# Performance work log

Measured on AMD Instinct MI355X. Metric: run time of the kernel, lower is better.

## Reference

```python
import jax, jax.numpy as jnp
import numpy as np
import math

NUM_HEADS = 8
HEAD_DIM = 64
MID = NUM_HEADS * HEAD_DIM  # 512
OUT_FEATURES = 512
NUM_BUCKETS = 32            # rel_pos_num_buckets (module passes 2*this to bucket fn)
MAX_DISTANCE = 128
SCALE = HEAD_DIM ** -0.5


def _relative_position_bucket(rel_pos, num_buckets, max_distance):
    # faithful port of RelativePositionBias._relative_position_bucket
    num_buckets = num_buckets // 2
    ret = (rel_pos >= 0).astype(jnp.int32) * num_buckets
    n = jnp.abs(rel_pos)
    max_exact = max(1, num_buckets // 2)
    denom = math.log(max_distance / max_exact) if max_distance > max_exact else 1.0
    n_float = jnp.maximum(n.astype(jnp.float32), 1.0)
    val_if_large = (max_exact + jnp.log(n_float / max_exact) / denom * (num_buckets - max_exact)).astype(jnp.int32)
    val_if_large = jnp.minimum(val_if_large, num_buckets - 1)
    ret = ret + jnp.where(n < max_exact, n, val_if_large)
    return ret


def rel_pos_bias(table, num_q, num_k):
    # table: [2*NUM_BUCKETS, heads] -> bias [1, heads, q, k]
    q_pos = jnp.arange(num_q, dtype=jnp.int32)
    k_pos = jnp.arange(num_k, dtype=jnp.int32)
    rel = k_pos[None, :] - q_pos[:, None]                      # [q, k]
    bucket = _relative_position_bucket(rel, NUM_BUCKETS * 2, MAX_DISTANCE)
    bias = table[bucket]                                       # [q, k, h]
    return jnp.transpose(bias, (2, 0, 1))[None]                # [1, h, q, k]


def setup_inputs() -> dict:
    key = jax.random.key(0)
    ks = jax.random.split(key, 6)
    b, n = 2, 4096
    q = jax.random.normal(ks[0], (b, n, MID), dtype=jnp.float32)
    k = jax.random.normal(ks[1], (b, n, MID), dtype=jnp.float32)
    v = jax.random.normal(ks[2], (b, n, MID), dtype=jnp.float32)
    # bucket indices range over [0, 2*NUM_BUCKETS); size table accordingly
    rel_bias_table = jax.random.normal(ks[3], (2 * NUM_BUCKETS, NUM_HEADS), dtype=jnp.float32) * 0.02
    W_out = jax.random.normal(ks[4], (MID, OUT_FEATURES), dtype=jnp.float32) * (1.0 / math.sqrt(MID))
    b_out = jax.random.normal(ks[5], (OUT_FEATURES,), dtype=jnp.float32) * 0.01
    return {"q": q, "k": k, "v": v, "rel_bias_table": rel_bias_table, "W_out": W_out, "b_out": b_out}


def reference(q, k, v, rel_bias_table, W_out, b_out):
    b, n, _ = q.shape
    m = k.shape[1]
    split = lambda t: jnp.transpose(t.reshape(t.shape[0], t.shape[1], NUM_HEADS, HEAD_DIM), (0, 2, 1, 3))
    qh, kh, vh = split(q), split(k), split(v)                  # [b, h, n, d]
    sim = jnp.einsum('bhnd,bhmd->bhnm', qh, kh)                # [b, h, n, m]
    sim = sim + rel_pos_bias(rel_bias_table, n, m)             # bias added BEFORE scaling (as in source)
    sim = sim * SCALE
    attn = jax.nn.softmax(sim, axis=-1)
    out = jnp.einsum('bhnm,bhmd->bhnd', attn, vh)              # [b, h, n, d]
    out = jnp.transpose(out, (0, 2, 1, 3)).reshape(b, n, MID)  # [b, n, h*d]
    return out @ W_out + b_out
```

## Files before the change

kernel.cpp:

```cpp
#include <hip/hip_runtime.h>
#include <hip/hip_bf16.h>
#include <math.h>

#define BB 2
#define HH 8
#define NN 4096
#define DD 64
#define MID 512
#define NOUT 512
#define QB 128
#define KVT 64
#define NT (NN / KVT)
#define LOG2E 1.44269504088896340736f
#define SCALE 0.125f

typedef __attribute__((ext_vector_type(8)))  short bf16x8;
typedef __attribute__((ext_vector_type(4)))  float f32x4;
typedef __attribute__((ext_vector_type(16))) float f32x16;

__device__ __forceinline__ short f2bf(float x) {
  unsigned u = __builtin_bit_cast(unsigned, x);
  u = (u + 0x7FFFu + ((u >> 16) & 1u)) >> 16;
  return (short)u;
}

__device__ __forceinline__ int rp_bucket(int rel) {
  int ret = (rel >= 0) ? 32 : 0;
  int n = (rel >= 0) ? rel : -rel;
  if (n < 16) return ret + n;
  float nf = (float)n;
  float vf = 16.0f + (logf(nf * (1.0f / 16.0f)) / 2.0794415416798357f) * 16.0f;
  int vi = (int)vf;
  vi = vi < 31 ? vi : 31;
  return ret + vi;
}

__device__ __forceinline__ unsigned cvtpk(float lo, float hi) {
  unsigned d;
  asm("v_cvt_pk_bf16_f32 %0, %1, %2" : "=v"(d) : "v"(lo), "v"(hi));
  return d;
}

__device__ __forceinline__ void gl2lds16(const void* g, void* l) {
  __builtin_amdgcn_global_load_lds(
      (const __attribute__((address_space(1))) unsigned*)g,
      (__attribute__((address_space(3))) unsigned*)l, 16, 0, 0);
}

__global__ __launch_bounds__(256) void prep_kernel(
    const float* __restrict__ W,  short* __restrict__ Wt,
    const float* __restrict__ K,  short* __restrict__ Kws,
    const float* __restrict__ V,  short* __restrict__ Vtws)
{
  const int bx = blockIdx.x;
  const int t  = threadIdx.x;
  if (bx < 2048) {
    int i = bx * 256 + t;
    int a = i & 7;
    int h = (i >> 3) & 7;
    int n = (i >> 6) & 4095;
    int b = i >> 18;
    const float* src = K + ((size_t)(b * 4096 + n) * 512 + h * 64 + a * 8);
    float4 x0 = *(const float4*)src;
    float4 x1 = *(const float4*)(src + 4);
    union { unsigned u[4]; bf16x8 v; } pk;
    pk.u[0] = cvtpk(x0.x, x0.y); pk.u[1] = cvtpk(x0.z, x0.w);
    pk.u[2] = cvtpk(x1.x, x1.y); pk.u[3] = cvtpk(x1.z, x1.w);
    size_t off = ((size_t)(b * 8 + h) * 4096 + n) * 64 + (size_t)((a ^ (n & 7)) * 8);
    *(bf16x8*)(Kws + off) = pk.v;
  } else if (bx < 3072) {
    __shared__ short Vl[64][72];
    const int idx = bx - 2048;
    const int g = idx & 63;
    const int bh = idx >> 6;
    const int b = bh >> 3, h = bh & 7;
    const int c4 = t & 15, r = t >> 4;
    #pragma unroll
    for (int rr = 0; rr < 4; ++rr) {
      int nl = r + rr * 16;
      const float* src = V + ((size_t)(b * 4096 + g * 64 + nl) * 512 + h * 64 + c4 * 4);
      float4 x = *(const float4*)src;
      unsigned lo = cvtpk(x.x, x.y), hi2 = cvtpk(x.z, x.w);
      unsigned* dst = (unsigned*)&Vl[nl][c4 * 4];
      dst[0] = lo; dst[1] = hi2;
    }
    __syncthreads();
    #pragma unroll
    for (int it = 0; it < 2; ++it) {
      int u = t + it * 256;
      int d = u >> 3, sp = u & 7;
      int s = sp ^ (d & 7);
      union { short s[8]; bf16x8 v; } pk;
      #pragma unroll
      for (int e = 0; e < 8; ++e) {
        int np  = s * 8 + e;
        int p16 = np & 15;
        int kvl = (np & 48) | (4 * (p16 >> 3) + (p16 & 3) + 8 * ((p16 >> 2) & 1));
        pk.s[e] = Vl[kvl][d];
      }
      *(bf16x8*)(Vtws + ((size_t)bh * 64 + d) * 4096 + g * 64 + sp * 8) = pk.v;
    }
  } else {
    __shared__ short Wl[64][72];
    const int idx = bx - 3072;
    const int k0 = (idx & 7) * 64;
    const int n0 = (idx >> 3) * 64;
    const int c4 = t & 15, r = t >> 4;
    #pragma unroll
    for (int rr = 0; rr < 4; ++rr) {
      int kl = r + rr * 16;
      const float* src = W + (size_t)(k0 + kl) * 512 + n0 + c4 * 4;
      float4 x = *(const float4*)src;
      unsigned lo = cvtpk(x.x, x.y), hi2 = cvtpk(x.z, x.w);
      unsigned* dst = (unsigned*)&Wl[kl][c4 * 4];
      dst[0] = lo; dst[1] = hi2;
    }
    __syncthreads();
    #pragma unroll
    for (int it = 0; it < 2; ++it) {
      int u = t + it * 256;
      int nl = u >> 3, a = u & 7;
      union { short s[8]; bf16x8 v; } pk;
      #pragma unroll
      for (int e = 0; e < 8; ++e) pk.s[e] = Wl[a * 8 + e][nl];
      *(bf16x8*)(Wt + (size_t)(n0 + nl) * 512 + k0 + a * 8) = pk.v;
    }
  }
}

__global__ __launch_bounds__(256, 2) void attn_kernel(
    const float* __restrict__ q, const short* __restrict__ kws,
    const short* __restrict__ vtws, const float* __restrict__ table,
    short* __restrict__ attn_out)
{
  __shared__ short Ks[3][4096];
  __shared__ short Vs[3][4096];
  __shared__ float biasb[512];
  __shared__ float Lw[4][32];

  const int tid = threadIdx.x;
  const int w   = tid >> 6;
  const int l   = tid & 63;
  const int lq  = l & 31;
  const int hi  = l >> 5;

  const int raw = blockIdx.x;
  const int bh  = (raw & 7) * 2 + (raw >> 8);
  const int xb  = (raw >> 3) & 31;
  const int b = bh >> 3, h = bh & 7;
  const int q0 = xb * QB;
  const int qw = q0 + w * 32;
  const int qg = qw + lq;

  const float smul = SCALE * LOG2E;

  for (int i = tid; i < 512; i += 256)
    biasb[i] = table[rp_bucket(i - 256) * HH + h] * smul;
  const float c_lo = table[31 * HH + h] * smul;
  const float c_hi = table[63 * HH + h] * smul;

  f32x16 c16h, c16l;
  #pragma unroll
  for (int r = 0; r < 16; ++r) { c16h[r] = c_hi; c16l[r] = c_lo; }

  bf16x8 qf[4];
  {
    const float* qr = q + ((size_t)b * NN + qg) * MID + (size_t)h * DD;
    #pragma unroll
    for (int dc = 0; dc < 4; ++dc) {
      int d0 = dc * 16 + hi * 8;
      float4 a0 = *(const float4*)(qr + d0);
      float4 a1 = *(const float4*)(qr + d0 + 4);
      bf16x8 f;
      f[0] = f2bf(a0.x * smul); f[1] = f2bf(a0.y * smul);
      f[2] = f2bf(a0.z * smul); f[3] = f2bf(a0.w * smul);
      f[4] = f2bf(a1.x * smul); f[5] = f2bf(a1.y * smul);
      f[6] = f2bf(a1.z * smul); f[7] = f2bf(a1.w * smul);
      qf[dc] = f;
    }
  }

  const short* kbh = kws  + (size_t)bh * NN * DD;
  const short* vbh = vtws + (size_t)bh * DD * NN;

  f32x16 o0a = {}, o0b = {}, o1a = {}, o1b = {};
  float ls0 = 0.f, ls1 = 0.f, ls2 = 0.f, ls3 = 0.f;

  const int o1w = w * 1024 + l * 16;
  const int o2w = o1w + 4096;
  const char* pkA = (const char*)kbh + o1w;
  const char* pvA = (const char*)vbh + (size_t)(o1w >> 7) * 8192 + (o1w & 127);
  const char* pvB = (const char*)vbh + (size_t)(o2w >> 7) * 8192 + (o2w & 127);
  char* ldsK = (char*)&Ks[0][0] + w * 1024;
  char* ldsV = (char*)&Vs[0][0] + w * 1024;
  const char* kbase = (const char*)&Ks[0][0];
  const char* vbase = (const char*)&Vs[0][0];

#define STAGE(BOFF) {                                   \
    gl2lds16(pkA,        ldsK + (BOFF));                \
    gl2lds16(pkA + 4096, ldsK + (BOFF) + 4096);         \
    gl2lds16(pvA,        ldsV + (BOFF));                \
    gl2lds16(pvB,        ldsV + (BOFF) + 4096);         \
    pkA += 8192; pvA += 128; pvB += 128; }

  __syncthreads();
  STAGE(0);
  STAGE(8192);

  int bo_cur = 0, bo_nxt = 16384;

  for (int t = 0; t < NT; ++t) {
    if (t + 1 < NT) asm volatile("s_waitcnt vmcnt(4)" ::: "memory");
    else            asm volatile("s_waitcnt vmcnt(0)" ::: "memory");
    __builtin_amdgcn_s_barrier();

    const int kv0 = t * KVT;

    const char* kr0 = kbase + bo_cur + lq * 128;
    const char* kr1 = kr0 + 32 * 128;
    const int swz = lq & 7;
    bf16x8 kf00 = *(const bf16x8*)(kr0 + ((hi ^ swz) << 4));
    bf16x8 kf10 = *(const bf16x8*)(kr1 + ((hi ^ swz) << 4));

    const int lo_rel = kv0 - (qw + 31);
    const int hi_rel = kv0 + KVT - 1 - qw;
    f32x16 acc0, acc1;
    if (lo_rel > 127) {
      acc0 = __builtin_amdgcn_mfma_f32_32x32x16_bf16(kf00, qf[0], c16h, 0, 0, 0);
      acc1 = __builtin_amdgcn_mfma_f32_32x32x16_bf16(kf10, qf[0], c16h, 0, 0, 0);
    } else if (hi_rel < -127) {
      acc0 = __builtin_amdgcn_mfma_f32_32x32x16_bf16(kf00, qf[0], c16l, 0, 0, 0);
      acc1 = __builtin_amdgcn_mfma_f32_32x32x16_bf16(kf10, qf[0], c16l, 0, 0, 0);
    } else {
      const int bidx0 = kv0 - qg + 256;
      f32x16 g0, g1;
      #pragma unroll
      for (int r = 0; r < 16; ++r) {
        int cr = (r & 3) + 8 * (r >> 2) + 4 * hi;
        g0[r] = biasb[bidx0 + cr];
        g1[r] = biasb[bidx0 + 32 + cr];
      }
      acc0 = __builtin_amdgcn_mfma_f32_32x32x16_bf16(kf00, qf[0], g0, 0, 0, 0);
      acc1 = __builtin_amdgcn_mfma_f32_32x32x16_bf16(kf10, qf[0], g1, 0, 0, 0);
    }
    __builtin_amdgcn_s_setprio(1);
    #pragma unroll
    for (int dc = 1; dc < 4; ++dc) {
      bf16x8 kf0 = *(const bf16x8*)(kr0 + (((dc * 2 + hi) ^ swz) << 4));
      bf16x8 kf1 = *(const bf16x8*)(kr1 + (((dc * 2 + hi) ^ swz) << 4));
      acc0 = __builtin_amdgcn_mfma_f32_32x32x16_bf16(kf0, qf[dc], acc0, 0, 0, 0);
      acc1 = __builtin_amdgcn_mfma_f32_32x32x16_bf16(kf1, qf[dc], acc1, 0, 0, 0);
    }
    __builtin_amdgcn_s_setprio(0);

    float p0[16], p1[16];
    #pragma unroll
    for (int r = 0; r < 16; ++r) p0[r] = __builtin_amdgcn_exp2f(acc0[r]);
    #pragma unroll
    for (int r = 0; r < 16; ++r) p1[r] = __builtin_amdgcn_exp2f(acc1[r]);

    ls0 += ((p0[0] + p0[1]) + (p0[2] + p0[3])) + ((p0[4] + p0[5]) + (p0[6] + p0[7]));
    ls1 += ((p0[8] + p0[9]) + (p0[10] + p0[11])) + ((p0[12] + p0[13]) + (p0[14] + p0[15]));
    ls2 += ((p1[0] + p1[1]) + (p1[2] + p1[3])) + ((p1[4] + p1[5]) + (p1[6] + p1[7]));
    ls3 += ((p1[8] + p1[9]) + (p1[10] + p1[11])) + ((p1[12] + p1[13]) + (p1[14] + p1[15]));

    bf16x8 pa[4];
    {
      union { unsigned u[4]; bf16x8 v; } ua, ub, uc, ud;
      ua.u[0] = cvtpk(p0[0],  p0[1]);  ua.u[1] = cvtpk(p0[2],  p0[3]);
      ua.u[2] = cvtpk(p0[4],  p0[5]);  ua.u[3] = cvtpk(p0[6],  p0[7]);
      ub.u[0] = cvtpk(p0[8],  p0[9]);  ub.u[1] = cvtpk(p0[10], p0[11]);
      ub.u[2] = cvtpk(p0[12], p0[13]); ub.u[3] = cvtpk(p0[14], p0[15]);
      uc.u[0] = cvtpk(p1[0],  p1[1]);  uc.u[1] = cvtpk(p1[2],  p1[3]);
      uc.u[2] = cvtpk(p1[4],  p1[5]);  uc.u[3] = cvtpk(p1[6],  p1[7]);
      ud.u[0] = cvtpk(p1[8],  p1[9]);  ud.u[1] = cvtpk(p1[10], p1[11]);
      ud.u[2] = cvtpk(p1[12], p1[13]); ud.u[3] = cvtpk(p1[14], p1[15]);
      pa[0] = ua.v; pa[1] = ub.v; pa[2] = uc.v; pa[3] = ud.v;
    }

    {
      const char* vr0 = vbase + bo_cur + lq * 128;
      const char* vr1 = vr0 + 32 * 128;
      const int s0 = lq & 7;
      __builtin_amdgcn_s_setprio(1);
      #pragma unroll
      for (int ks = 0; ks < 4; ks += 2) {
        bf16x8 vfa0 = *(const bf16x8*)(vr0 + (((hi + 2 * ks) ^ s0) << 4));
        bf16x8 vfb0 = *(const bf16x8*)(vr0 + (((hi + 2 * (ks + 1)) ^ s0) << 4));
        bf16x8 vfa1 = *(const bf16x8*)(vr1 + (((hi + 2 * ks) ^ s0) << 4));
        bf16x8 vfb1 = *(const bf16x8*)(vr1 + (((hi + 2 * (ks + 1)) ^ s0) << 4));
        o0a = __builtin_amdgcn_mfma_f32_32x32x16_bf16(pa[ks],     vfa0, o0a, 0, 0, 0);
        o0b = __builtin_amdgcn_mfma_f32_32x32x16_bf16(pa[ks + 1], vfb0, o0b, 0, 0, 0);
        o1a = __builtin_amdgcn_mfma_f32_32x32x16_bf16(pa[ks],     vfa1, o1a, 0, 0, 0);
        o1b = __builtin_amdgcn_mfma_f32_32x32x16_bf16(pa[ks + 1], vfb1, o1b, 0, 0, 0);
      }
      __builtin_amdgcn_s_setprio(0);
    }

    if (t + 2 < NT) STAGE(bo_nxt);
    bo_cur = (bo_cur == 16384) ? 0 : bo_cur + 8192;
    bo_nxt = (bo_nxt == 16384) ? 0 : bo_nxt + 8192;
  }

  f32x16 o0, o1;
  #pragma unroll
  for (int r = 0; r < 16; ++r) { o0[r] = o0a[r] + o0b[r]; o1[r] = o1a[r] + o1b[r]; }
  float lsum = (ls0 + ls1) + (ls2 + ls3);
  float tot = lsum + __shfl_xor(lsum, 32);
  if (l < 32) Lw[w][l] = tot;
  __syncthreads();
  float inv[16];
  #pragma unroll
  for (int g = 0; g < 4; ++g) {
    f32x4 t4 = *(const f32x4*)&Lw[w][g * 8 + hi * 4];
    inv[g * 4 + 0] = 1.0f / t4[0];
    inv[g * 4 + 1] = 1.0f / t4[1];
    inv[g * 4 + 2] = 1.0f / t4[2];
    inv[g * 4 + 3] = 1.0f / t4[3];
  }
  const size_t ob = ((size_t)b * NN + qw) * MID + (size_t)h * DD;
  #pragma unroll
  for (int r = 0; r < 16; ++r) {
    const int crow = (r & 3) + 8 * (r >> 2) + 4 * hi;
    short* orow = attn_out + ob + (size_t)crow * MID;
    orow[lq]      = f2bf(o0[r] * inv[r]);
    orow[32 + lq] = f2bf(o1[r] * inv[r]);
  }
#undef STAGE
}

__global__ __launch_bounds__(256) void proj_kernel(
    const short* __restrict__ A, const short* __restrict__ Wt,
    const float* __restrict__ bias, float* __restrict__ out)
{
  const int tid = threadIdx.x;
  const int w  = tid >> 6;
  const int l  = tid & 63;
  const int lr = l & 15;
  const int lg = l >> 4;
  const int m0 = blockIdx.x * 64 + w * 16;
  const int n0 = blockIdx.y * 64;

  f32x4 acc[4] = {};
  const short* ar = A + (size_t)(m0 + lr) * MID + lg * 8;
  #pragma unroll
  for (int kk = 0; kk < MID; kk += 32) {
    bf16x8 af = *(const bf16x8*)(ar + kk);
    #pragma unroll
    for (int u = 0; u < 4; ++u) {
      bf16x8 bfr = *(const bf16x8*)(Wt + (size_t)(n0 + u * 16 + lr) * MID + kk + lg * 8);
      acc[u] = __builtin_amdgcn_mfma_f32_16x16x32_bf16(af, bfr, acc[u], 0, 0, 0);
    }
  }
  #pragma unroll
  for (int u = 0; u < 4; ++u) {
    float bb = bias[n0 + u * 16 + lr];
    #pragma unroll
    for (int r = 0; r < 4; ++r)
      out[(size_t)(m0 + lg * 4 + r) * NOUT + n0 + u * 16 + lr] = acc[u][r] + bb;
  }
}

extern "C" void kernel_launch(void* const* d_in, const int* in_sizes, int n_in,
                              void* d_out, int out_size, void* d_ws, size_t ws_size,
                              hipStream_t stream) {
  const float* q     = (const float*)d_in[0];
  const float* k     = (const float*)d_in[1];
  const float* v     = (const float*)d_in[2];
  const float* table = (const float*)d_in[3];
  const float* W     = (const float*)d_in[4];
  const float* bo    = (const float*)d_in[5];
  float* out = (float*)d_out;

  char* wsp = (char*)d_ws;
  short* attn_ws = (short*)wsp;                       wsp += (size_t)BB * NN * MID * 2;
  short* Wt      = (short*)wsp;                       wsp += (size_t)MID * NOUT * 2;
  short* kws     = (short*)wsp;                       wsp += (size_t)BB * HH * NN * DD * 2;
  short* vtws    = (short*)wsp;

  hipLaunchKernelGGL(prep_kernel, dim3(3136), dim3(256), 0, stream,
                     W, Wt, k, kws, v, vtws);
  hipLaunchKernelGGL(attn_kernel, dim3(BB * HH * (NN / QB)), dim3(256), 0, stream,
                     q, kws, vtws, table, attn_ws);
  hipLaunchKernelGGL(proj_kernel, dim3(BB * NN / 64, NOUT / 64), dim3(256), 0, stream,
                     attn_ws, Wt, bo, out);
}
```

Before: 132.2 us.

## Software-pipeline PV matmul one tile behind QK and remap projection grid

The attention loop now runs the P·V MFMAs for the previous KV tile at the top of each iteration, after the barrier, so that PV work can overlap with the next tile's QK and softmax. This needs a fourth LDS buffer for K and V, giving a 4-slot ring with wraparound offsets. The LDS footprint grows by 16KB, which may limit occupancy at 2 blocks per CU. Separately, the projection kernel uses a flattened 1D grid with a swizzled block-to-tile mapping, intended to improve L2 locality.

New measurement: 134.0 us. About the same (+1.3%).

```diff
diff --git a/kernel.cpp b/kernel.cpp
--- a/kernel.cpp
+++ b/kernel.cpp
@@ -133,8 +133,8 @@
     const short* __restrict__ vtws, const float* __restrict__ table,
     short* __restrict__ attn_out)
 {
-  __shared__ short Ks[3][4096];
-  __shared__ short Vs[3][4096];
+  __shared__ short Ks[4][4096];
+  __shared__ short Vs[4][4096];
   __shared__ float biasb[512];
   __shared__ float Lw[4][32];
 
@@ -195,6 +195,9 @@
   char* ldsV = (char*)&Vs[0][0] + w * 1024;
   const char* kbase = (const char*)&Ks[0][0];
   const char* vbase = (const char*)&Vs[0][0];
+  const int swz = lq & 7;
+
+  bf16x8 pa0, pa1, pa2, pa3;
 
 #define STAGE(BOFF) {                                   \
     gl2lds16(pkA,        ldsK + (BOFF));                \
@@ -203,22 +206,47 @@
     gl2lds16(pvB,        ldsV + (BOFF) + 4096);         \
     pkA += 8192; pvA += 128; pvB += 128; }
 
-  __syncthreads();
+#define PVSTEP(BOFF) {                                                       \
+    const char* vr0 = vbase + (BOFF) + lq * 128;                             \
+    const char* vr1 = vr0 + 32 * 128;                                        \
+    __builtin_amdgcn_s_setprio(1);                                           \
+    bf16x8 vfa0 = *(const bf16x8*)(vr0 + (((hi + 0) ^ swz) << 4));           \
+    bf16x8 vfb0 = *(const bf16x8*)(vr0 + (((hi + 2) ^ swz) << 4));           \
+    bf16x8 vfa1 = *(const bf16x8*)(vr1 + (((hi + 0) ^ swz) << 4));           \
+    bf16x8 vfb1 = *(const bf16x8*)(vr1 + (((hi + 2) ^ swz) << 4));           \
+    o0a = __builtin_amdgcn_mfma_f32_32x32x16_bf16(pa0, vfa0, o0a, 0, 0, 0);  \
+    o0b = __builtin_amdgcn_mfma_f32_32x32x16_bf16(pa1, vfb0, o0b, 0, 0, 0);  \
+    o1a = __builtin_amdgcn_mfma_f32_32x32x16_bf16(pa0, vfa1, o1a, 0, 0, 0);  \
+    o1b = __builtin_amdgcn_mfma_f32_32x32x16_bf16(pa1, vfb1, o1b, 0, 0, 0);  \
+    bf16x8 vfa2 = *(const bf16x8*)(vr0 + (((hi + 4) ^ swz) << 4));           \
+    bf16x8 vfb2 = *(const bf16x8*)(vr0 + (((hi + 6) ^ swz) << 4));           \
+    bf16x8 vfa3 = *(const bf16x8*)(vr1 + (((hi + 4) ^ swz) << 4));           \
+    bf16x8 vfb3 = *(const bf16x8*)(vr1 + (((hi + 6) ^ swz) << 4));           \
+    o0a = __builtin_amdgcn_mfma_f32_32x32x16_bf16(pa2, vfa2, o0a, 0, 0, 0);  \
+    o0b = __builtin_amdgcn_mfma_f32_32x32x16_bf16(pa3, vfb2, o0b, 0, 0, 0);  \
+    o1a = __builtin_amdgcn_mfma_f32_32x32x16_bf16(pa2, vfa3, o1a, 0, 0, 0);  \
+    o1b = __builtin_amdgcn_mfma_f32_32x32x16_bf16(pa3, vfb3, o1b, 0, 0, 0);  \
+    __builtin_amdgcn_s_setprio(0); }
+
   STAGE(0);
   STAGE(8192);
-
-  int bo_cur = 0, bo_nxt = 16384;
+  __syncthreads();
+
+  int bo    = 0;
+  int bo_st = 16384;
 
   for (int t = 0; t < NT; ++t) {
-    if (t + 1 < NT) asm volatile("s_waitcnt vmcnt(4)" ::: "memory");
-    else            asm volatile("s_waitcnt vmcnt(0)" ::: "memory");
-    __builtin_amdgcn_s_barrier();
+    if (t) {
+      if (t + 1 < NT) asm volatile("s_waitcnt vmcnt(4)" ::: "memory");
+      else            asm volatile("s_waitcnt vmcnt(0)" ::: "memory");
+      __builtin_amdgcn_s_barrier();
+      PVSTEP((bo + 24576) & 32767);
+    }
 
     const int kv0 = t * KVT;
 
-    const char* kr0 = kbase + bo_cur + lq * 128;
+    const char* kr0 = kbase + bo + lq * 128;
     const char* kr1 = kr0 + 32 * 128;
-    const int swz = lq & 7;
     bf16x8 kf00 = *(const bf16x8*)(kr0 + ((hi ^ swz) << 4));
     bf16x8 kf10 = *(const bf16x8*)(kr1 + ((hi ^ swz) << 4));
 
@@ -264,7 +292,6 @@
     ls2 += ((p1[0] + p1[1]) + (p1[2] + p1[3])) + ((p1[4] + p1[5]) + (p1[6] + p1[7]));
     ls3 += ((p1[8] + p1[9]) + (p1[10] + p1[11])) + ((p1[12] + p1[13]) + (p1[14] + p1[15]));
 
-    bf16x8 pa[4];
     {
       union { unsigned u[4]; bf16x8 v; } ua, ub, uc, ud;
       ua.u[0] = cvtpk(p0[0],  p0[1]);  ua.u[1] = cvtpk(p0[2],  p0[3]);
@@ -275,32 +302,15 @@
       uc.u[2] = cvtpk(p1[4],  p1[5]);  uc.u[3] = cvtpk(p1[6],  p1[7]);
       ud.u[0] = cvtpk(p1[8],  p1[9]);  ud.u[1] = cvtpk(p1[10], p1[11]);
       ud.u[2] = cvtpk(p1[12], p1[13]); ud.u[3] = cvtpk(p1[14], p1[15]);
-      pa[0] = ua.v; pa[1] = ub.v; pa[2] = uc.v; pa[3] = ud.v;
-    }
-
-    {
-      const char* vr0 = vbase + bo_cur + lq * 128;
-      const char* vr1 = vr0 + 32 * 128;
-      const int s0 = lq & 7;
-      __builtin_amdgcn_s_setprio(1);
-      #pragma unroll
-      for (int ks = 0; ks < 4; ks += 2) {
-        bf16x8 vfa0 = *(const bf16x8*)(vr0 + (((hi + 2 * ks) ^ s0) << 4));
-        bf16x8 vfb0 = *(const bf16x8*)(vr0 + (((hi + 2 * (ks + 1)) ^ s0) << 4));
-        bf16x8 vfa1 = *(const bf16x8*)(vr1 + (((hi + 2 * ks) ^ s0) << 4));
-        bf16x8 vfb1 = *(const bf16x8*)(vr1 + (((hi + 2 * (ks + 1)) ^ s0) << 4));
-        o0a = __builtin_amdgcn_mfma_f32_32x32x16_bf16(pa[ks],     vfa0, o0a, 0, 0, 0);
-        o0b = __builtin_amdgcn_mfma_f32_32x32x16_bf16(pa[ks + 1], vfb0, o0b, 0, 0, 0);
-        o1a = __builtin_amdgcn_mfma_f32_32x32x16_bf16(pa[ks],     vfa1, o1a, 0, 0, 0);
-        o1b = __builtin_amdgcn_mfma_f32_32x32x16_bf16(pa[ks + 1], vfb1, o1b, 0, 0, 0);
-      }
-      __builtin_amdgcn_s_setprio(0);
-    }
-
-    if (t + 2 < NT) STAGE(bo_nxt);
-    bo_cur = (bo_cur == 16384) ? 0 : bo_cur + 8192;
-    bo_nxt = (bo_nxt == 16384) ? 0 : bo_nxt + 8192;
-  }
+      pa0 = ua.v; pa1 = ub.v; pa2 = uc.v; pa3 = ud.v;
+    }
+
+    if (t + 2 < NT) { STAGE(bo_st); }
+    bo_st = (bo_st + 8192) & 32767;
+    bo    = (bo + 8192) & 32767;
+  }
+
+  PVSTEP((bo + 24576) & 32767);
 
   f32x16 o0, o1;
   #pragma unroll
@@ -327,6 +337,7 @@
     orow[32 + lq] = f2bf(o1[r] * inv[r]);
   }
 #undef STAGE
+#undef PVSTEP
 }
 
 __global__ __launch_bounds__(256) void proj_kernel(
@@ -338,8 +349,10 @@
   const int l  = tid & 63;
   const int lr = l & 15;
   const int lg = l >> 4;
-  const int m0 = blockIdx.x * 64 + w * 16;
-  const int n0 = blockIdx.y * 64;
+  const int bid = blockIdx.x;
+  const int mt = (bid & 7) * 16 + ((bid >> 3) & 15);
+  const int n0 = (bid >> 7) * 64;
+  const int m0 = mt * 64 + w * 16;
 
   f32x4 acc[4] = {};
   const short* ar = A + (size_t)(m0 + lr) * MID + lg * 8;
@@ -382,6 +395,6 @@
                      W, Wt, k, kws, v, vtws);
   hipLaunchKernelGGL(attn_kernel, dim3(BB * HH * (NN / QB)), dim3(256), 0, stream,
                      q, kws, vtws, table, attn_ws);
-  hipLaunchKernelGGL(proj_kernel, dim3(BB * NN / 64, NOUT / 64), dim3(256), 0, stream,
+  hipLaunchKernelGGL(proj_kernel, dim3(BB * NN / 64 * (NOUT / 64)), dim3(256), 0, stream,
                      attn_ws, Wt, bo, out);
 }
```
